# Performance work log

Measured on AMD Instinct MI355X. Metric: run time of the kernel, lower is better.

The kernel has to match this reference:

```python
import jax, jax.numpy as jnp
import numpy as np

B, C, H, Wd = 4, 64, 64, 64


def setup_inputs() -> dict:
    key = jax.random.key(0)
    k1, k2, k3 = jax.random.split(key, 3)
    x = jax.random.normal(k1, (B, C, H, Wd), dtype=jnp.float32)
    W = jax.random.normal(k2, (C, C), dtype=jnp.float32) * (1.0 / np.sqrt(C))
    b = jax.random.normal(k3, (C,), dtype=jnp.float32) * 0.01
    return {"x": x, "W": W, "b": b}


def reference(x, W, b):
    Bz, Cz, Hz, Wz = x.shape
    N = Hz * Wz
    xf = x.reshape(Bz, Cz, N)                      # values [B,C,N]
    # shared 1x1 conv for queries and keys (same module instance in torch)
    qk = jnp.einsum('oc,bcn->bon', W, xf) + b[None, :, None]  # [B,C,N]
    # scores[b,n,m] = sum_c q[b,c,n] * k[b,c,m], scaled by 1/N
    scores = jnp.einsum('bcn,bcm->bnm', qk, qk) / N           # [B,N,N]
    attn = jax.nn.softmax(scores, axis=-1)                    # softmax over m
    # out[b,c,n] = sum_m values[b,c,m] * attn[b,n,m]
    out = jnp.einsum('bcm,bnm->bcn', xf, attn)
    return out.reshape(Bz, Cz, Hz, Wz)
```

## Files before the change

kernel.cpp:

```cpp
#include <hip/hip_runtime.h>
#include <hip/hip_bf16.h>

#define BATCH 4
#define NSP   4096

#define QKSCALE 0.0187675376f

typedef __bf16 bf16x8v __attribute__((ext_vector_type(8)));
typedef __bf16 bf16x4v __attribute__((ext_vector_type(4)));
typedef float  floatx4 __attribute__((ext_vector_type(4)));
typedef float  floatx16 __attribute__((ext_vector_type(16)));
typedef unsigned uivec2 __attribute__((ext_vector_type(2)));

static __device__ __forceinline__ float fast_exp2(float x) {
#if __has_builtin(__builtin_amdgcn_exp2f)
    return __builtin_amdgcn_exp2f(x);
#else
    return exp2f(x);
#endif
}

static __device__ __forceinline__ unsigned pkbf(float a, float b) {
    union { __bf16 h[2]; unsigned u; } x;
    x.h[0] = (__bf16)a; x.h[1] = (__bf16)b;
    return x.u;
}

static __device__ __forceinline__ void plswap(unsigned &a, unsigned &b) {
#if __has_builtin(__builtin_amdgcn_permlane32_swap)
    uivec2 r = __builtin_amdgcn_permlane32_swap(a, b, false, false);
    a = r[0]; b = r[1];
#else
    asm("v_permlane32_swap_b32 %0, %1" : "+v"(a), "+v"(b));
#endif
}

__global__ __launch_bounds__(256) void qk_kernel(const float* __restrict__ x,
                                                 const float* __restrict__ Wm,
                                                 const float* __restrict__ bias,
                                                 __bf16* __restrict__ qkT,
                                                 __bf16* __restrict__ xbf) {
    __shared__ __align__(16) __bf16 xT[64 * 72];

    const int t  = threadIdx.x;
    const int b  = blockIdx.x >> 6;
    const int n0 = (blockIdx.x & 63) << 6;

#pragma unroll
    for (int p = 0; p < 4; ++p) {
        const int c  = p * 16 + (t >> 4);
        const int n4 = (t & 15) * 4;
        const float4 v = *(const float4*)(x + (size_t)(b * 64 + c) * 4096 + n0 + n4);
        xT[(n4 + 0) * 72 + c] = (__bf16)(v.x * QKSCALE);
        xT[(n4 + 1) * 72 + c] = (__bf16)(v.y * QKSCALE);
        xT[(n4 + 2) * 72 + c] = (__bf16)(v.z * QKSCALE);
        xT[(n4 + 3) * 72 + c] = (__bf16)(v.w * QKSCALE);
        bf16x4v xv;
        xv[0] = (__bf16)v.x; xv[1] = (__bf16)v.y; xv[2] = (__bf16)v.z; xv[3] = (__bf16)v.w;
        *(bf16x4v*)(xbf + (size_t)(b * 64 + c) * 4096 + n0 + n4) = xv;
    }
    __syncthreads();

    const int w = t >> 6, lane = t & 63, quad = lane >> 4, l16 = lane & 15;
    const bf16x8v a0 = *(const bf16x8v*)(xT + (w * 16 + l16) * 72 + quad * 8);
    const bf16x8v a1 = *(const bf16x8v*)(xT + (w * 16 + l16) * 72 + 32 + quad * 8);

    floatx4 acc[4];
#pragma unroll
    for (int ot = 0; ot < 4; ++ot) {
        const float* wr = Wm + (ot * 16 + l16) * 64;
        float4 wa = *(const float4*)(wr + quad * 8);
        float4 wb = *(const float4*)(wr + quad * 8 + 4);
        float4 wc = *(const float4*)(wr + 32 + quad * 8);
        float4 wd = *(const float4*)(wr + 32 + quad * 8 + 4);
        bf16x8v b0, b1;
        b0[0]=(__bf16)wa.x; b0[1]=(__bf16)wa.y; b0[2]=(__bf16)wa.z; b0[3]=(__bf16)wa.w;
        b0[4]=(__bf16)wb.x; b0[5]=(__bf16)wb.y; b0[6]=(__bf16)wb.z; b0[7]=(__bf16)wb.w;
        b1[0]=(__bf16)wc.x; b1[1]=(__bf16)wc.y; b1[2]=(__bf16)wc.z; b1[3]=(__bf16)wc.w;
        b1[4]=(__bf16)wd.x; b1[5]=(__bf16)wd.y; b1[6]=(__bf16)wd.z; b1[7]=(__bf16)wd.w;
        acc[ot] = floatx4{0.f, 0.f, 0.f, 0.f};
        acc[ot] = __builtin_amdgcn_mfma_f32_16x16x32_bf16(a0, b0, acc[ot], 0, 0, 0);
        acc[ot] = __builtin_amdgcn_mfma_f32_16x16x32_bf16(a1, b1, acc[ot], 0, 0, 0);
    }
    __syncthreads();

#pragma unroll
    for (int ot = 0; ot < 4; ++ot) {
        const float bo = bias[ot * 16 + l16] * QKSCALE;
#pragma unroll
        for (int r = 0; r < 4; ++r)
            xT[(w * 16 + quad * 4 + r) * 72 + ot * 16 + l16] = (__bf16)(acc[ot][r] + bo);
    }
    __syncthreads();

    const int n = t >> 2, seg = t & 3;
    __bf16* dst = qkT + (size_t)(b * 4096 + n0 + n) * 64 + seg * 16;
    *(bf16x8v*)dst       = *(const bf16x8v*)(xT + n * 72 + seg * 16);
    *(bf16x8v*)(dst + 8) = *(const bf16x8v*)(xT + n * 72 + seg * 16 + 8);
}

template<int SPLIT, int ITERS>
__global__ __launch_bounds__(512, 4) void attn_kernel(const __bf16* __restrict__ xbf,
                                                      const __bf16* __restrict__ qkT,
                                                      __bf16* __restrict__ Opart,
                                                      float* __restrict__ Lpart) {
    __shared__ __align__(16) char smem[33280];
    __bf16* Klds  = (__bf16*)smem;
    __bf16* Vlds  = (__bf16*)(smem + 16384);
    __bf16* Oldsb = (__bf16*)smem;

    const int t   = threadIdx.x;
    const int blk = blockIdx.x;
    const int xcd = blk & 7;
    const int b   = xcd >> 1;
    const int sub = ((blk >> 3) << 1) | (xcd & 1);
    const int qt  = sub / SPLIT;
    const int s   = sub % SPLIT;
    const int n0  = qt << 8;
    const int pblk = (b * 16 + qt) * SPLIT + s;

    const int w = t >> 6, lane = t & 63, l31 = lane & 31, hi = lane >> 5;

    const __bf16* kgl = qkT + (size_t)b * 4096 * 64;
    const __bf16* vgl = xbf + (size_t)b * 64 * 4096;

    bf16x8v qf[4];
    {
        const __bf16* qrow = kgl + (size_t)(n0 + w * 32 + l31) * 64;
#pragma unroll
        for (int kb = 0; kb < 4; ++kb)
            qf[kb] = *(const bf16x8v*)(qrow + kb * 16 + hi * 8);
    }

    floatx16 oacc[2] = {};
    float rs = 0.f;

    const int srow = t >> 3;
    const int scol = t & 7;
    const int slot = ((scol ^ (srow & 7)) * 8);
    uint4 kst, vst;
    auto stage_load = [&](int m0) {
        kst = *(const uint4*)(kgl + (size_t)(m0 + srow) * 64 + scol * 8);
        vst = *(const uint4*)(vgl + (size_t)srow * 4096 + m0 + scol * 8);
    };
    auto stage_write = [&](int buf) {
        *(uint4*)(Klds + buf * 4096 + srow * 64 + slot) = kst;
        *(uint4*)(Vlds + buf * 4096 + srow * 64 + slot) = vst;
    };

    const int mbase = s * (64 * ITERS);
    stage_load(mbase);
    stage_write(0);
    int cur = 0;

    for (int it = 0; it < ITERS; ++it) {
        __syncthreads();
        if (it + 1 < ITERS)
            stage_load(mbase + ((it + 1) << 6));
        const __bf16* Kc = Klds + cur * 4096;
        const __bf16* Vc = Vlds + cur * 4096;

        __builtin_amdgcn_s_setprio(1);
#pragma unroll
        for (int mt = 0; mt < 2; ++mt) {
            bf16x8v kf[4];
#pragma unroll
            for (int kb = 0; kb < 4; ++kb)
                kf[kb] = *(const bf16x8v*)(Kc + (mt * 32 + l31) * 64 +
                                           (((kb * 2 + hi) ^ (l31 & 7)) * 8));

            bf16x8v vf[2][2];
#pragma unroll
            for (int ct = 0; ct < 2; ++ct)
#pragma unroll
                for (int ks = 0; ks < 2; ++ks)
                    vf[ct][ks] = *(const bf16x8v*)(Vc + (ct * 32 + l31) * 64 +
                                                   (((mt * 4 + ks * 2 + hi) ^ (l31 & 7)) * 8));

            floatx16 acc = {};
#pragma unroll
            for (int kb = 0; kb < 4; ++kb)
                acc = __builtin_amdgcn_mfma_f32_32x32x16_bf16(kf[kb], qf[kb], acc, 0, 0, 0);

            unsigned wdx[8];
            float sum = 0.f;
#pragma unroll
            for (int i = 0; i < 8; ++i) {
                float e0 = fast_exp2(acc[2 * i]);
                float e1 = fast_exp2(acc[2 * i + 1]);
                sum += e0 + e1;
                wdx[i] = pkbf(e0, e1);
            }
            rs += sum;

            plswap(wdx[0], wdx[2]);
            plswap(wdx[1], wdx[3]);
            plswap(wdx[4], wdx[6]);
            plswap(wdx[5], wdx[7]);
            union { unsigned u[4]; bf16x8v v; } pb0, pb1;
            pb0.u[0] = wdx[0]; pb0.u[1] = wdx[1]; pb0.u[2] = wdx[2]; pb0.u[3] = wdx[3];
            pb1.u[0] = wdx[4]; pb1.u[1] = wdx[5]; pb1.u[2] = wdx[6]; pb1.u[3] = wdx[7];

#pragma unroll
            for (int ct = 0; ct < 2; ++ct) {
                oacc[ct] = __builtin_amdgcn_mfma_f32_32x32x16_bf16(vf[ct][0], pb0.v, oacc[ct], 0, 0, 0);
                oacc[ct] = __builtin_amdgcn_mfma_f32_32x32x16_bf16(vf[ct][1], pb1.v, oacc[ct], 0, 0, 0);
            }
        }
        __builtin_amdgcn_s_setprio(0);

        if (it + 1 < ITERS) stage_write(cur ^ 1);
        cur ^= 1;
    }

    {
        float v = rs + __shfl_xor(rs, 32, 64);
        if (lane < 32)
            Lpart[(size_t)pblk * 256 + w * 32 + l31] = v;
    }

    __syncthreads();

#pragma unroll
    for (int ct = 0; ct < 2; ++ct)
#pragma unroll
        for (int r = 0; r < 16; ++r) {
            const int c = ct * 32 + (r & 3) + 8 * (r >> 2) + 4 * hi;
            Oldsb[c * 260 + w * 32 + l31] = (__bf16)oacc[ct][r];
        }
    __syncthreads();

    const int c = t >> 3, qs = (t & 7) * 32;
#pragma unroll
    for (int i = 0; i < 4; ++i)
        *(bf16x8v*)(Opart + (size_t)pblk * 16384 + c * 256 + qs + i * 8) =
            *(const bf16x8v*)(Oldsb + c * 260 + qs + i * 8);
}

template<int SPLIT>
__global__ __launch_bounds__(256) void reduce_kernel(const __bf16* __restrict__ Opart,
                                                     const float* __restrict__ Lpart,
                                                     float* __restrict__ out) {
    const int blk = blockIdx.x;
    const int bq = blk >> 3, cq = blk & 7;
    const int b = bq >> 4, qt = bq & 15;
    const int t = threadIdx.x;
    const int c  = cq * 8 + (t >> 5);
    const int q8 = (t & 31) * 8;

    float l[8] = {0.f,0.f,0.f,0.f,0.f,0.f,0.f,0.f};
#pragma unroll
    for (int s = 0; s < SPLIT; ++s) {
        const float* lp = Lpart + ((size_t)bq * SPLIT + s) * 256 + q8;
        float4 u = *(const float4*)lp;
        float4 v = *(const float4*)(lp + 4);
        l[0]+=u.x; l[1]+=u.y; l[2]+=u.z; l[3]+=u.w;
        l[4]+=v.x; l[5]+=v.y; l[6]+=v.z; l[7]+=v.w;
    }
    float a[8] = {0.f,0.f,0.f,0.f,0.f,0.f,0.f,0.f};
#pragma unroll
    for (int s = 0; s < SPLIT; ++s) {
        bf16x8v v = *(const bf16x8v*)(Opart + ((size_t)bq * SPLIT + s) * 16384 + c * 256 + q8);
#pragma unroll
        for (int k = 0; k < 8; ++k) a[k] += (float)v[k];
    }
    float* op = out + (size_t)(b * 64 + c) * 4096 + qt * 256 + q8;
    float4 o0, o1;
    o0.x = a[0]/l[0]; o0.y = a[1]/l[1]; o0.z = a[2]/l[2]; o0.w = a[3]/l[3];
    o1.x = a[4]/l[4]; o1.y = a[5]/l[5]; o1.z = a[6]/l[6]; o1.w = a[7]/l[7];
    *(float4*)op       = o0;
    *(float4*)(op + 4) = o1;
}

extern "C" void kernel_launch(void* const* d_in, const int* in_sizes, int n_in,
                              void* d_out, int out_size, void* d_ws, size_t ws_size,
                              hipStream_t stream) {
    const float* x    = (const float*)d_in[0];
    const float* Wm   = (const float*)d_in[1];
    const float* bias = (const float*)d_in[2];
    float* out = (float*)d_out;

    char* ws = (char*)d_ws;
    __bf16* qkT = (__bf16*)ws;
    __bf16* xbf = (__bf16*)(ws + 2097152);
    const size_t HEAD = 2097152 + 2097152;

    qk_kernel<<<BATCH * (NSP / 64), 256, 0, stream>>>(x, Wm, bias, qkT, xbf);

    const size_t need16 = HEAD + (size_t)1024 * 16384 * 2 + (size_t)1024 * 256 * 4;
    const size_t need8  = HEAD + (size_t)512  * 16384 * 2 + (size_t)512  * 256 * 4;
    if (ws_size >= need16) {
        __bf16* Opart = (__bf16*)(ws + HEAD);
        float*  Lpart = (float*)(ws + HEAD + (size_t)1024 * 16384 * 2);
        attn_kernel<16, 4><<<BATCH * 16 * 16, 512, 0, stream>>>(xbf, qkT, Opart, Lpart);
        reduce_kernel<16><<<512, 256, 0, stream>>>(Opart, Lpart, out);
    } else if (ws_size >= need8) {
        __bf16* Opart = (__bf16*)(ws + HEAD);
        float*  Lpart = (float*)(ws + HEAD + (size_t)512 * 16384 * 2);
        attn_kernel<8, 8><<<BATCH * 16 * 8, 512, 0, stream>>>(xbf, qkT, Opart, Lpart);
        reduce_kernel<8><<<512, 256, 0, stream>>>(Opart, Lpart, out);
    } else {
        __bf16* Opart = (__bf16*)(ws + HEAD);
        float*  Lpart = (float*)(ws + HEAD + (size_t)256 * 16384 * 2);
        attn_kernel<4, 16><<<BATCH * 16 * 4, 512, 0, stream>>>(xbf, qkT, Opart, Lpart);
        reduce_kernel<4><<<512, 256, 0, stream>>>(Opart, Lpart, out);
    }
}
```

Baseline: 101.9 us.

## Load whole 256-key chunk into LDS at once instead of double-buffered 64-key pipeline

The attention kernel now stages an entire 256-key chunk of K and V into a 64KB LDS buffer in one burst, then runs four unrolled 64-key compute steps from LDS with no interleaved prefetch. This replaces the double-buffered per-64-key register-staged pipeline and its per-iteration barriers. The s_setprio raise is narrowed so it covers only the MFMA groups, and the SPLIT=8 fallback is dropped. The cost is doubled LDS per block, which likely caps occupancy below the launch-bounds target, and global loads no longer overlap with compute inside a block.

```diff
diff --git a/kernel.cpp b/kernel.cpp
--- a/kernel.cpp
+++ b/kernel.cpp
@@ -99,14 +99,14 @@
     *(bf16x8v*)(dst + 8) = *(const bf16x8v*)(xT + n * 72 + seg * 16 + 8);
 }
 
-template<int SPLIT, int ITERS>
+template<int SPLIT, int NCHUNK>
 __global__ __launch_bounds__(512, 4) void attn_kernel(const __bf16* __restrict__ xbf,
                                                       const __bf16* __restrict__ qkT,
                                                       __bf16* __restrict__ Opart,
                                                       float* __restrict__ Lpart) {
-    __shared__ __align__(16) char smem[33280];
+    __shared__ __align__(16) char smem[65536];
     __bf16* Klds  = (__bf16*)smem;
-    __bf16* Vlds  = (__bf16*)(smem + 16384);
+    __bf16* Vlds  = (__bf16*)(smem + 32768);
     __bf16* Oldsb = (__bf16*)smem;
 
     const int t   = threadIdx.x;
@@ -137,80 +137,80 @@
 
     const int srow = t >> 3;
     const int scol = t & 7;
-    const int slot = ((scol ^ (srow & 7)) * 8);
-    uint4 kst, vst;
-    auto stage_load = [&](int m0) {
-        kst = *(const uint4*)(kgl + (size_t)(m0 + srow) * 64 + scol * 8);
-        vst = *(const uint4*)(vgl + (size_t)srow * 4096 + m0 + scol * 8);
-    };
-    auto stage_write = [&](int buf) {
-        *(uint4*)(Klds + buf * 4096 + srow * 64 + slot) = kst;
-        *(uint4*)(Vlds + buf * 4096 + srow * 64 + slot) = vst;
-    };
-
-    const int mbase = s * (64 * ITERS);
-    stage_load(mbase);
-    stage_write(0);
-    int cur = 0;
-
-    for (int it = 0; it < ITERS; ++it) {
+    const int kslot = (scol ^ (srow & 7)) * 8;
+
+    for (int ch = 0; ch < NCHUNK; ++ch) {
+        const int m0 = (s * NCHUNK + ch) * 256;
+
+        if (ch) __syncthreads();
+        uint4 kreg[4], vreg[4];
+#pragma unroll
+        for (int i = 0; i < 4; ++i)
+            kreg[i] = *(const uint4*)(kgl + (size_t)(m0 + i * 64 + srow) * 64 + scol * 8);
+#pragma unroll
+        for (int i = 0; i < 4; ++i)
+            vreg[i] = *(const uint4*)(vgl + (size_t)srow * 4096 + m0 + (i * 8 + scol) * 8);
+#pragma unroll
+        for (int i = 0; i < 4; ++i)
+            *(uint4*)(Klds + (i * 64 + srow) * 64 + kslot) = kreg[i];
+#pragma unroll
+        for (int i = 0; i < 4; ++i)
+            *(uint4*)(Vlds + srow * 256 + i * 64 + kslot) = vreg[i];
         __syncthreads();
-        if (it + 1 < ITERS)
-            stage_load(mbase + ((it + 1) << 6));
-        const __bf16* Kc = Klds + cur * 4096;
-        const __bf16* Vc = Vlds + cur * 4096;
-
-        __builtin_amdgcn_s_setprio(1);
-#pragma unroll
-        for (int mt = 0; mt < 2; ++mt) {
-            bf16x8v kf[4];
-#pragma unroll
-            for (int kb = 0; kb < 4; ++kb)
-                kf[kb] = *(const bf16x8v*)(Kc + (mt * 32 + l31) * 64 +
-                                           (((kb * 2 + hi) ^ (l31 & 7)) * 8));
-
-            bf16x8v vf[2][2];
-#pragma unroll
-            for (int ct = 0; ct < 2; ++ct)
-#pragma unroll
-                for (int ks = 0; ks < 2; ++ks)
-                    vf[ct][ks] = *(const bf16x8v*)(Vc + (ct * 32 + l31) * 64 +
-                                                   (((mt * 4 + ks * 2 + hi) ^ (l31 & 7)) * 8));
-
-            floatx16 acc = {};
-#pragma unroll
-            for (int kb = 0; kb < 4; ++kb)
-                acc = __builtin_amdgcn_mfma_f32_32x32x16_bf16(kf[kb], qf[kb], acc, 0, 0, 0);
-
-            unsigned wdx[8];
-            float sum = 0.f;
-#pragma unroll
-            for (int i = 0; i < 8; ++i) {
-                float e0 = fast_exp2(acc[2 * i]);
-                float e1 = fast_exp2(acc[2 * i + 1]);
-                sum += e0 + e1;
-                wdx[i] = pkbf(e0, e1);
-            }
-            rs += sum;
-
-            plswap(wdx[0], wdx[2]);
-            plswap(wdx[1], wdx[3]);
-            plswap(wdx[4], wdx[6]);
-            plswap(wdx[5], wdx[7]);
-            union { unsigned u[4]; bf16x8v v; } pb0, pb1;
-            pb0.u[0] = wdx[0]; pb0.u[1] = wdx[1]; pb0.u[2] = wdx[2]; pb0.u[3] = wdx[3];
-            pb1.u[0] = wdx[4]; pb1.u[1] = wdx[5]; pb1.u[2] = wdx[6]; pb1.u[3] = wdx[7];
-
-#pragma unroll
-            for (int ct = 0; ct < 2; ++ct) {
-                oacc[ct] = __builtin_amdgcn_mfma_f32_32x32x16_bf16(vf[ct][0], pb0.v, oacc[ct], 0, 0, 0);
-                oacc[ct] = __builtin_amdgcn_mfma_f32_32x32x16_bf16(vf[ct][1], pb1.v, oacc[ct], 0, 0, 0);
+
+#pragma unroll
+        for (int it = 0; it < 4; ++it) {
+#pragma unroll
+            for (int mt = 0; mt < 2; ++mt) {
+                bf16x8v kf[4];
+#pragma unroll
+                for (int kb = 0; kb < 4; ++kb)
+                    kf[kb] = *(const bf16x8v*)(Klds + (it * 64 + mt * 32 + l31) * 64 +
+                                               (((kb * 2 + hi) ^ (l31 & 7)) * 8));
+
+                bf16x8v vf[2][2];
+#pragma unroll
+                for (int ct = 0; ct < 2; ++ct)
+#pragma unroll
+                    for (int ks = 0; ks < 2; ++ks)
+                        vf[ct][ks] = *(const bf16x8v*)(Vlds + (ct * 32 + l31) * 256 + it * 64 +
+                                                       (((mt * 4 + ks * 2 + hi) ^ (l31 & 7)) * 8));
+
+                __builtin_amdgcn_s_setprio(1);
+                floatx16 acc = {};
+#pragma unroll
+                for (int kb = 0; kb < 4; ++kb)
+                    acc = __builtin_amdgcn_mfma_f32_32x32x16_bf16(kf[kb], qf[kb], acc, 0, 0, 0);
+                __builtin_amdgcn_s_setprio(0);
+
+                unsigned wdx[8];
+                float sum = 0.f;
+#pragma unroll
+                for (int i = 0; i < 8; ++i) {
+                    float e0 = fast_exp2(acc[2 * i]);
+                    float e1 = fast_exp2(acc[2 * i + 1]);
+                    sum += e0 + e1;
+                    wdx[i] = pkbf(e0, e1);
+                }
+                rs += sum;
+
+                plswap(wdx[0], wdx[2]);
+                plswap(wdx[1], wdx[3]);
+                plswap(wdx[4], wdx[6]);
+                plswap(wdx[5], wdx[7]);
+                union { unsigned u[4]; bf16x8v v; } pb0, pb1;
+                pb0.u[0] = wdx[0]; pb0.u[1] = wdx[1]; pb0.u[2] = wdx[2]; pb0.u[3] = wdx[3];
+                pb1.u[0] = wdx[4]; pb1.u[1] = wdx[5]; pb1.u[2] = wdx[6]; pb1.u[3] = wdx[7];
+
+                __builtin_amdgcn_s_setprio(1);
+#pragma unroll
+                for (int ct = 0; ct < 2; ++ct) {
+                    oacc[ct] = __builtin_amdgcn_mfma_f32_32x32x16_bf16(vf[ct][0], pb0.v, oacc[ct], 0, 0, 0);
+                    oacc[ct] = __builtin_amdgcn_mfma_f32_32x32x16_bf16(vf[ct][1], pb1.v, oacc[ct], 0, 0, 0);
+                }
+                __builtin_amdgcn_s_setprio(0);
             }
         }
-        __builtin_amdgcn_s_setprio(0);
-
-        if (it + 1 < ITERS) stage_write(cur ^ 1);
-        cur ^= 1;
     }
 
     {
@@ -288,21 +288,15 @@
     qk_kernel<<<BATCH * (NSP / 64), 256, 0, stream>>>(x, Wm, bias, qkT, xbf);
 
     const size_t need16 = HEAD + (size_t)1024 * 16384 * 2 + (size_t)1024 * 256 * 4;
-    const size_t need8  = HEAD + (size_t)512  * 16384 * 2 + (size_t)512  * 256 * 4;
     if (ws_size >= need16) {
         __bf16* Opart = (__bf16*)(ws + HEAD);
         float*  Lpart = (float*)(ws + HEAD + (size_t)1024 * 16384 * 2);
-        attn_kernel<16, 4><<<BATCH * 16 * 16, 512, 0, stream>>>(xbf, qkT, Opart, Lpart);
+        attn_kernel<16, 1><<<BATCH * 16 * 16, 512, 0, stream>>>(xbf, qkT, Opart, Lpart);
         reduce_kernel<16><<<512, 256, 0, stream>>>(Opart, Lpart, out);
-    } else if (ws_size >= need8) {
-        __bf16* Opart = (__bf16*)(ws + HEAD);
-        float*  Lpart = (float*)(ws + HEAD + (size_t)512 * 16384 * 2);
-        attn_kernel<8, 8><<<BATCH * 16 * 8, 512, 0, stream>>>(xbf, qkT, Opart, Lpart);
-        reduce_kernel<8><<<512, 256, 0, stream>>>(Opart, Lpart, out);
     } else {
         __bf16* Opart = (__bf16*)(ws + HEAD);
         float*  Lpart = (float*)(ws + HEAD + (size_t)256 * 16384 * 2);
-        attn_kernel<4, 16><<<BATCH * 16 * 4, 512, 0, stream>>>(xbf, qkT, Opart, Lpart);
+        attn_kernel<4, 4><<<BATCH * 16 * 4, 512, 0, stream>>>(xbf, qkT, Opart, Lpart);
         reduce_kernel<4><<<512, 256, 0, stream>>>(Opart, Lpart, out);
     }
 }
```

Measured after the change: 98.66 us. 3.2% less time.
